# Kernel tuning notes

Hardware: AMD Instinct MI355X
Metric: run time of the kernel (lower is better)

Reference implementation:

```python
import jax, jax.numpy as jnp
import numpy as np

B, S, D, H, E, K = 4, 2048, 1024, 4096, 8, 2


def setup_inputs() -> dict:
    key = jax.random.key(0)
    ks = jax.random.split(key, 7)
    sd = 1.0 / np.sqrt(D)
    sh = 1.0 / np.sqrt(H)
    return {
        "x": jax.random.normal(ks[0], (B, S, D), dtype=jnp.float32),
        "Wg": jax.random.uniform(ks[1], (D, E), jnp.float32, -sd, sd),
        "bg": jnp.zeros((E,), jnp.float32),
        "W1": jax.random.uniform(ks[2], (E, D, H), jnp.float32, -sd, sd),
        "b1": jax.random.uniform(ks[3], (E, H), jnp.float32, -sd, sd),
        "W2": jax.random.uniform(ks[4], (E, H, D), jnp.float32, -sh, sh),
        "b2": jax.random.uniform(ks[5], (E, D), jnp.float32, -sh, sh),
    }


def reference(x, Wg, bg, W1, b1, W2, b2):
    # gating: softmax over experts, then top-k
    probs = jax.nn.softmax(x @ Wg + bg, axis=-1)            # [B,S,E]
    topv, topi = jax.lax.top_k(probs, K)                     # [B,S,K]
    # NOTE: original computes normalized scores but uses RAW top-k scores
    # scatter raw top-k scores back to dense per-expert weights [B,S,E]
    onehot = jax.nn.one_hot(topi, E, dtype=x.dtype)          # [B,S,K,E]
    w_dense = jnp.einsum("bske,bsk->bse", onehot, topv)      # [B,S,E]
    out = jnp.zeros_like(x)
    for e in range(E):
        h = jax.nn.relu(jnp.einsum("bsd,dh->bsh", x, W1[e]) + b1[e])
        y = jnp.einsum("bsh,hd->bsd", h, W2[e]) + b2[e]
        out = out + y * w_dense[..., e:e + 1]
    return out
```

## Files before the change

### kernel.cpp

```cpp
#include <hip/hip_runtime.h>

typedef unsigned short u16;
typedef __attribute__((ext_vector_type(8))) short bf16x8;
typedef __attribute__((ext_vector_type(8))) unsigned short u16x8;
typedef __attribute__((ext_vector_type(4))) float f32x4;

#define NTOK 8192
#define DDIM 1024
#define HDIM 4096
#define NEXP 8

typedef __attribute__((address_space(1))) const void gvoid;
typedef __attribute__((address_space(3))) void lvoid;

__device__ __forceinline__ u16 f2b(float f) {
  unsigned u = __float_as_uint(f);
  u += 0x7fffu + ((u >> 16) & 1u);
  return (u16)(u >> 16);
}
__device__ __forceinline__ void glds16(const void* g, void* l) {
  __builtin_amdgcn_global_load_lds((gvoid*)g, (lvoid*)l, 16, 0, 0);
}

__global__ void convert_x_kernel(const float* __restrict__ src, u16* __restrict__ dst) {
  size_t i = ((size_t)blockIdx.x * 256 + threadIdx.x) * 8;
  float4 a = *(const float4*)(src + i);
  float4 b = *(const float4*)(src + i + 4);
  u16x8 o;
  o[0] = f2b(a.x); o[1] = f2b(a.y); o[2] = f2b(a.z); o[3] = f2b(a.w);
  o[4] = f2b(b.x); o[5] = f2b(b.y); o[6] = f2b(b.z); o[7] = f2b(b.w);
  *(u16x8*)(dst + i) = o;
}

__global__ void transpose_kernel(const float* __restrict__ src, u16* __restrict__ dst,
                                 int R, int C) {
  int e = blockIdx.z;
  src += (size_t)e * R * C;
  dst += (size_t)e * R * C;
  int r0 = blockIdx.y * 64, c0 = blockIdx.x * 64;
  __shared__ u16 T[64][68];
  int t = threadIdx.x;
  int rr = t >> 4, cc = (t & 15) * 4;
#pragma unroll
  for (int i = 0; i < 4; ++i) {
    int r = i * 16 + rr;
    float4 v = *(const float4*)(src + (size_t)(r0 + r) * C + c0 + cc);
    T[cc + 0][r] = f2b(v.x);
    T[cc + 1][r] = f2b(v.y);
    T[cc + 2][r] = f2b(v.z);
    T[cc + 3][r] = f2b(v.w);
  }
  __syncthreads();
#pragma unroll
  for (int i = 0; i < 4; ++i) {
    int c = i * 16 + rr;
    ushort4 o = *(const ushort4*)&T[c][cc];
    *(ushort4*)(dst + (size_t)(c0 + c) * R + r0 + cc) = o;
  }
}

__global__ void gate_kernel(const float* __restrict__ x, const float* __restrict__ Wg,
                            const float* __restrict__ bg, int* __restrict__ counts_pad,
                            int* __restrict__ pair_tok, float* __restrict__ pair_w,
                            int* __restrict__ tok_ep)
{
  int lane = threadIdx.x & 63;
  int wave = threadIdx.x >> 6;
  int tok = blockIdx.x * 4 + wave;
  const float* xr = x + (size_t)tok * DDIM + lane * 16;
  float acc[NEXP];
#pragma unroll
  for (int e = 0; e < NEXP; ++e) acc[e] = 0.f;
#pragma unroll
  for (int j = 0; j < 16; ++j) {
    float xf = xr[j];
    const float* wr = Wg + (size_t)(lane * 16 + j) * NEXP;
    float4 wa = *(const float4*)(wr);
    float4 wb = *(const float4*)(wr + 4);
    acc[0] = fmaf(xf, wa.x, acc[0]);
    acc[1] = fmaf(xf, wa.y, acc[1]);
    acc[2] = fmaf(xf, wa.z, acc[2]);
    acc[3] = fmaf(xf, wa.w, acc[3]);
    acc[4] = fmaf(xf, wb.x, acc[4]);
    acc[5] = fmaf(xf, wb.y, acc[5]);
    acc[6] = fmaf(xf, wb.z, acc[6]);
    acc[7] = fmaf(xf, wb.w, acc[7]);
  }
#pragma unroll
  for (int off = 32; off > 0; off >>= 1) {
#pragma unroll
    for (int e = 0; e < NEXP; ++e) acc[e] += __shfl_xor(acc[e], off, 64);
  }
  if (lane == 0) {
    float l[NEXP];
    float mx = -3.4e38f;
#pragma unroll
    for (int e = 0; e < NEXP; ++e) { l[e] = acc[e] + bg[e]; mx = fmaxf(mx, l[e]); }
    float s = 0.f;
#pragma unroll
    for (int e = 0; e < NEXP; ++e) { l[e] = __expf(l[e] - mx); s += l[e]; }
    float inv = 1.f / s;
    float v1 = -1.f; int i1 = 0;
#pragma unroll
    for (int e = 0; e < NEXP; ++e) { if (l[e] > v1) { v1 = l[e]; i1 = e; } }
    float v2 = -1.f; int i2 = 0;
#pragma unroll
    for (int e = 0; e < NEXP; ++e) { if (e != i1 && l[e] > v2) { v2 = l[e]; i2 = e; } }
    int p1 = atomicAdd(&counts_pad[i1 * 32], 1);
    pair_tok[i1 * NTOK + p1] = tok;
    pair_w[i1 * NTOK + p1] = v1 * inv;
    tok_ep[2 * tok + 0] = (i1 << 16) | p1;
    int p2 = atomicAdd(&counts_pad[i2 * 32], 1);
    pair_tok[i2 * NTOK + p2] = tok;
    pair_w[i2 * NTOK + p2] = v2 * inv;
    tok_ep[2 * tok + 1] = (i2 << 16) | p2;
  }
}

__global__ void offsets_kernel(const int* __restrict__ counts_pad, int* __restrict__ counts,
                               int* __restrict__ offsets, int* __restrict__ tile_e,
                               int* __restrict__ tile_i0, int* __restrict__ ntiles)
{
  if (threadIdx.x == 0) {
    int s = 0;
    for (int e = 0; e < NEXP; ++e) {
      int c = counts_pad[e * 32];
      counts[e] = c; offsets[e] = s; s += c;
    }
    int nt_ = 0;
    for (int e = 0; e < NEXP; ++e)
      for (int i0 = 0; i0 < counts[e]; i0 += 128) { tile_e[nt_] = e; tile_i0[nt_] = i0; nt_++; }
    *ntiles = nt_;
  }
}

__device__ __forceinline__ void stage4(const u16* xa0, const u16* xa1,
                                       const u16* wb0, const u16* wb1,
                                       u16* Asb, u16* Bsb, int wave, int koff) {
  glds16(xa0 + koff, Asb + wave * 512);
  glds16(xa1 + koff, Asb + 2048 + wave * 512);
  glds16(wb0 + koff, Bsb + wave * 512);
  glds16(wb1 + koff, Bsb + 2048 + wave * 512);
}

__device__ __forceinline__ void mfma_tile(const u16* Asb, const u16* Bsb,
                                          f32x4 (&acc)[4][4],
                                          int wrr, int wc, int ln, int q) {
  bf16x8 af[4], bfr[4];
#pragma unroll
  for (int mt = 0; mt < 4; ++mt)
    af[mt] = *(const bf16x8*)(Asb + (wrr + mt * 16 + ln) * 32 + q * 8);
#pragma unroll
  for (int nt = 0; nt < 4; ++nt)
    bfr[nt] = *(const bf16x8*)(Bsb + (wc + nt * 16 + ln) * 32 + q * 8);
#pragma unroll
  for (int mt = 0; mt < 4; ++mt)
#pragma unroll
    for (int nt = 0; nt < 4; ++nt)
      acc[mt][nt] = __builtin_amdgcn_mfma_f32_16x16x32_bf16(af[mt], bfr[nt], acc[mt][nt], 0, 0, 0);
}

__global__ __launch_bounds__(256) void gemm1_kernel(
    const u16* __restrict__ xb, const u16* __restrict__ W1T,
    const float* __restrict__ b1, const int* __restrict__ counts,
    const int* __restrict__ offsets, const int* __restrict__ ntiles,
    const int* __restrict__ tile_e, const int* __restrict__ tile_i0,
    const int* __restrict__ pair_tok, u16* __restrict__ h, int hp, int p0)
{
  int bx = blockIdx.x;
  if (bx >= *ntiles) return;
  int e = tile_e[bx];
  int i0 = tile_i0[bx];
  int cnt = counts[e];
  int n0 = blockIdx.y * 128;

  __shared__ __align__(16) u16 As[2][128 * 32];
  __shared__ __align__(16) u16 Bs[2][128 * 32];

  int t = threadIdx.x;
  int lane = t & 63;
  int wave = t >> 6;
  int rlim = cnt - i0;
  int rl = rlim - 1;

  const int* tokp = pair_tok + e * NTOK + i0;
  int arow = t >> 2;
  int c8 = (t & 3) * 8;
  const u16* xa0 = xb + (size_t)tokp[min(arow, rl)] * DDIM + c8;
  const u16* xa1 = xb + (size_t)tokp[min(arow + 64, rl)] * DDIM + c8;
  const u16* wb0 = W1T + (size_t)e * HDIM * DDIM + (size_t)(p0 + n0 + arow) * DDIM + c8;
  const u16* wb1 = wb0 + (size_t)64 * DDIM;

  f32x4 acc[4][4] = {};
  int wrr = (wave >> 1) * 64;
  int wc = (wave & 1) * 64;
  int ln = lane & 15;
  int q = lane >> 4;

  stage4(xa0, xa1, wb0, wb1, As[0], Bs[0], wave, 0);
  __syncthreads();
  for (int k0 = 0; k0 < DDIM; k0 += 64) {
    stage4(xa0, xa1, wb0, wb1, As[1], Bs[1], wave, k0 + 32);
    __builtin_amdgcn_sched_barrier(0);
    mfma_tile(As[0], Bs[0], acc, wrr, wc, ln, q);
    __syncthreads();
    if (k0 + 64 < DDIM) {
      stage4(xa0, xa1, wb0, wb1, As[0], Bs[0], wave, k0 + 64);
      __builtin_amdgcn_sched_barrier(0);
    }
    mfma_tile(As[1], Bs[1], acc, wrr, wc, ln, q);
    __syncthreads();
  }

  int ob = offsets[e];
  float bb[4];
#pragma unroll
  for (int nt = 0; nt < 4; ++nt)
    bb[nt] = b1[(size_t)e * HDIM + p0 + n0 + wc + nt * 16 + ln];
  size_t hbase = (size_t)(ob + i0) * hp + n0 + wc;
#pragma unroll
  for (int mt = 0; mt < 4; ++mt) {
#pragma unroll
    for (int r = 0; r < 4; ++r) {
      int row = wrr + mt * 16 + q * 4 + r;
      if (row < rlim) {
        u16* hrow = h + hbase + (size_t)row * hp;
#pragma unroll
        for (int nt = 0; nt < 4; ++nt) {
          float v = acc[mt][nt][r] + bb[nt];
          hrow[nt * 16 + ln] = f2b(fmaxf(v, 0.f));
        }
      }
    }
  }
}

__global__ __launch_bounds__(256) void gemm2_kernel(
    const u16* __restrict__ h, const u16* __restrict__ W2T,
    const float* __restrict__ b2v, const int* __restrict__ counts,
    const int* __restrict__ offsets, const int* __restrict__ ntiles,
    const int* __restrict__ tile_e, const int* __restrict__ tile_i0,
    float* __restrict__ y, int hp, int p0, int first)
{
  int bx = blockIdx.x;
  if (bx >= *ntiles) return;
  int e = tile_e[bx];
  int i0 = tile_i0[bx];
  int cnt = counts[e];
  int n0 = blockIdx.y * 128;

  __shared__ __align__(16) u16 As[2][128 * 32];
  __shared__ __align__(16) u16 Bs[2][128 * 32];

  int t = threadIdx.x;
  int lane = t & 63;
  int wave = t >> 6;
  int rlim = cnt - i0;
  int rl = rlim - 1;
  int rbase = offsets[e] + i0;

  int arow = t >> 2;
  int c8 = (t & 3) * 8;
  const u16* xa0 = h + (size_t)(rbase + min(arow, rl)) * hp + c8;
  const u16* xa1 = h + (size_t)(rbase + min(arow + 64, rl)) * hp + c8;
  const u16* wb0 = W2T + (size_t)e * DDIM * HDIM + (size_t)(n0 + arow) * HDIM + p0 + c8;
  const u16* wb1 = wb0 + (size_t)64 * HDIM;

  f32x4 acc[4][4] = {};
  int wrr = (wave >> 1) * 64;
  int wc = (wave & 1) * 64;
  int ln = lane & 15;
  int q = lane >> 4;

  stage4(xa0, xa1, wb0, wb1, As[0], Bs[0], wave, 0);
  __syncthreads();
  for (int k0 = 0; k0 < hp; k0 += 64) {
    stage4(xa0, xa1, wb0, wb1, As[1], Bs[1], wave, k0 + 32);
    __builtin_amdgcn_sched_barrier(0);
    mfma_tile(As[0], Bs[0], acc, wrr, wc, ln, q);
    __syncthreads();
    if (k0 + 64 < hp) {
      stage4(xa0, xa1, wb0, wb1, As[0], Bs[0], wave, k0 + 64);
      __builtin_amdgcn_sched_barrier(0);
    }
    mfma_tile(As[1], Bs[1], acc, wrr, wc, ln, q);
    __syncthreads();
  }

  float bb[4];
#pragma unroll
  for (int nt = 0; nt < 4; ++nt)
    bb[nt] = first ? b2v[(size_t)e * DDIM + n0 + wc + nt * 16 + ln] : 0.f;
#pragma unroll
  for (int mt = 0; mt < 4; ++mt) {
#pragma unroll
    for (int r = 0; r < 4; ++r) {
      int row = wrr + mt * 16 + q * 4 + r;
      if (row < rlim) {
        float* yr = y + (size_t)(rbase + row) * DDIM + n0 + wc;
#pragma unroll
        for (int nt = 0; nt < 4; ++nt) {
          float v = acc[mt][nt][r] + bb[nt];
          if (first) yr[nt * 16 + ln] = v;
          else       yr[nt * 16 + ln] += v;
        }
      }
    }
  }
}

__global__ __launch_bounds__(256) void combine_kernel(
    const float* __restrict__ y, const int* __restrict__ tok_ep,
    const float* __restrict__ pair_w, const int* __restrict__ offsets,
    float* __restrict__ out)
{
  int tok = blockIdx.x;
  int ep1 = tok_ep[2 * tok + 0];
  int ep2 = tok_ep[2 * tok + 1];
  int e1 = ep1 >> 16, p1 = ep1 & 0xffff;
  int e2 = ep2 >> 16, p2 = ep2 & 0xffff;
  float w1 = pair_w[e1 * NTOK + p1];
  float w2 = pair_w[e2 * NTOK + p2];
  const float* r1 = y + (size_t)(offsets[e1] + p1) * DDIM;
  const float* r2 = y + (size_t)(offsets[e2] + p2) * DDIM;
  int c = threadIdx.x * 4;
  float4 a = *(const float4*)(r1 + c);
  float4 b = *(const float4*)(r2 + c);
  float4 o;
  o.x = w1 * a.x + w2 * b.x;
  o.y = w1 * a.y + w2 * b.y;
  o.z = w1 * a.z + w2 * b.z;
  o.w = w1 * a.w + w2 * b.w;
  *(float4*)(out + (size_t)tok * DDIM + c) = o;
}

extern "C" void kernel_launch(void* const* d_in, const int* in_sizes, int n_in,
                              void* d_out, int out_size, void* d_ws, size_t ws_size,
                              hipStream_t stream)
{
  const float* x  = (const float*)d_in[0];
  const float* Wg = (const float*)d_in[1];
  const float* bg = (const float*)d_in[2];
  const float* W1 = (const float*)d_in[3];
  const float* b1 = (const float*)d_in[4];
  const float* W2 = (const float*)d_in[5];
  const float* b2 = (const float*)d_in[6];
  float* out = (float*)d_out;

  char* ws = (char*)d_ws;
  int*   counts_pad = (int*)(ws + 0);
  int*   counts     = (int*)(ws + 1024);
  int*   offsets    = (int*)(ws + 1056);
  int*   ntiles     = (int*)(ws + 1088);
  int*   tile_e     = (int*)(ws + 1152);
  int*   tile_i0    = (int*)(ws + 2176);
  int*   tok_ep     = (int*)(ws + 4096);
  int*   pair_tok   = (int*)(ws + 69632);
  float* pair_w     = (float*)(ws + 331776);
  u16*   xb  = (u16*)(ws + 593920);
  u16*   W1T = (u16*)(ws + 593920 + 16777216);
  u16*   W2T = (u16*)(ws + 593920 + 16777216 + 67108864);
  float* yb  = (float*)(ws + 593920 + 16777216 + 2 * (size_t)67108864);
  u16*   hbuf = (u16*)(ws + 593920 + 16777216 + 3 * (size_t)67108864);
  size_t used_base = 593920 + 16777216 + 3 * (size_t)67108864;

  int hp = 256;
  const int cands[5] = {4096, 2048, 1024, 512, 256};
  for (int ci = 0; ci < 5; ++ci) {
    if (used_base + (size_t)16512 * cands[ci] * 2 <= ws_size) { hp = cands[ci]; break; }
  }

  hipMemsetAsync(counts_pad, 0, 1024, stream);
  convert_x_kernel<<<NTOK * DDIM / 2048, 256, 0, stream>>>(x, xb);
  transpose_kernel<<<dim3(HDIM / 64, DDIM / 64, NEXP), 256, 0, stream>>>(W1, W1T, DDIM, HDIM);
  transpose_kernel<<<dim3(DDIM / 64, HDIM / 64, NEXP), 256, 0, stream>>>(W2, W2T, HDIM, DDIM);
  gate_kernel<<<NTOK / 4, 256, 0, stream>>>(x, Wg, bg, counts_pad, pair_tok, pair_w, tok_ep);
  offsets_kernel<<<1, 64, 0, stream>>>(counts_pad, counts, offsets, tile_e, tile_i0, ntiles);
  for (int p0 = 0; p0 < HDIM; p0 += hp) {
    gemm1_kernel<<<dim3(136, hp / 128), 256, 0, stream>>>(
        xb, W1T, b1, counts, offsets, ntiles, tile_e, tile_i0, pair_tok, hbuf, hp, p0);
    gemm2_kernel<<<dim3(136, DDIM / 128), 256, 0, stream>>>(
        hbuf, W2T, b2, counts, offsets, ntiles, tile_e, tile_i0, yb, hp, p0, p0 == 0 ? 1 : 0);
  }
  combine_kernel<<<NTOK, 256, 0, stream>>>(yb, tok_ep, pair_w, offsets, out);
}
```

Measured before the change: 839.2 us.

## Triple-buffer GEMM K-loop with one barrier per step and interleave tile order

Replaces the double-buffered K loop in both expert GEMMs with a three-stage LDS ring. Each step waits on vmcnt so two loads stay in flight and uses a single s_barrier instead of two __syncthreads. The offsets kernel also permutes the tile list with a stride-17 interleave so blocks of different experts are mixed across the grid, marking padding slots with e=-1. This should hide global-to-LDS latency better and spread expert work more evenly, at the cost of 50% more LDS per block, which may lower occupancy.

```diff
diff --git a/kernel.cpp b/kernel.cpp
--- a/kernel.cpp
+++ b/kernel.cpp
@@ -9,6 +9,7 @@
 #define DDIM 1024
 #define HDIM 4096
 #define NEXP 8
+#define NTILE 136
 
 typedef __attribute__((address_space(1))) const void gvoid;
 typedef __attribute__((address_space(3))) void lvoid;
@@ -122,6 +123,7 @@
                                int* __restrict__ tile_i0, int* __restrict__ ntiles)
 {
   if (threadIdx.x == 0) {
+    int te[NTILE], ti[NTILE];
     int s = 0;
     for (int e = 0; e < NEXP; ++e) {
       int c = counts_pad[e * 32];
@@ -129,7 +131,12 @@
     }
     int nt_ = 0;
     for (int e = 0; e < NEXP; ++e)
-      for (int i0 = 0; i0 < counts[e]; i0 += 128) { tile_e[nt_] = e; tile_i0[nt_] = i0; nt_++; }
+      for (int i0 = 0; i0 < counts[e]; i0 += 128) { te[nt_] = e; ti[nt_] = i0; nt_++; }
+    for (int w = 0; w < NTILE; ++w) {
+      int t = (w & 7) * 17 + (w >> 3);
+      tile_e[w]  = (t < nt_) ? te[t] : -1;
+      tile_i0[w] = (t < nt_) ? ti[t] : 0;
+    }
     *ntiles = nt_;
   }
 }
@@ -160,6 +167,27 @@
       acc[mt][nt] = __builtin_amdgcn_mfma_f32_16x16x32_bf16(af[mt], bfr[nt], acc[mt][nt], 0, 0, 0);
 }
 
+#define GEMM_LOOP(KDIM)                                                      \
+  stage4(xa0, xa1, wb0, wb1, As[0], Bs[0], wave, 0);                         \
+  stage4(xa0, xa1, wb0, wb1, As[1], Bs[1], wave, 32);                        \
+  {                                                                          \
+    int cur = 0, nx2 = 2;                                                    \
+    for (int k0 = 0; k0 < (KDIM); k0 += 32) {                                \
+      __builtin_amdgcn_sched_barrier(0);                                     \
+      if (k0 + 32 < (KDIM))                                                  \
+        asm volatile("s_waitcnt vmcnt(4) lgkmcnt(0)" ::: "memory");          \
+      else                                                                   \
+        asm volatile("s_waitcnt vmcnt(0) lgkmcnt(0)" ::: "memory");          \
+      __builtin_amdgcn_s_barrier();                                          \
+      __builtin_amdgcn_sched_barrier(0);                                     \
+      if (k0 + 64 < (KDIM))                                                  \
+        stage4(xa0, xa1, wb0, wb1, As[nx2], Bs[nx2], wave, k0 + 64);         \
+      mfma_tile(As[cur], Bs[cur], acc, wrr, wc, ln, q);                      \
+      cur = (cur == 2) ? 0 : cur + 1;                                        \
+      nx2 = (nx2 == 2) ? 0 : nx2 + 1;                                        \
+    }                                                                        \
+  }
+
 __global__ __launch_bounds__(256) void gemm1_kernel(
     const u16* __restrict__ xb, const u16* __restrict__ W1T,
     const float* __restrict__ b1, const int* __restrict__ counts,
@@ -168,14 +196,14 @@
     const int* __restrict__ pair_tok, u16* __restrict__ h, int hp, int p0)
 {
   int bx = blockIdx.x;
-  if (bx >= *ntiles) return;
   int e = tile_e[bx];
+  if (e < 0) return;
   int i0 = tile_i0[bx];
   int cnt = counts[e];
   int n0 = blockIdx.y * 128;
 
-  __shared__ __align__(16) u16 As[2][128 * 32];
-  __shared__ __align__(16) u16 Bs[2][128 * 32];
+  __shared__ __align__(16) u16 As[3][4096];
+  __shared__ __align__(16) u16 Bs[3][4096];
 
   int t = threadIdx.x;
   int lane = t & 63;
@@ -197,20 +225,7 @@
   int ln = lane & 15;
   int q = lane >> 4;
 
-  stage4(xa0, xa1, wb0, wb1, As[0], Bs[0], wave, 0);
-  __syncthreads();
-  for (int k0 = 0; k0 < DDIM; k0 += 64) {
-    stage4(xa0, xa1, wb0, wb1, As[1], Bs[1], wave, k0 + 32);
-    __builtin_amdgcn_sched_barrier(0);
-    mfma_tile(As[0], Bs[0], acc, wrr, wc, ln, q);
-    __syncthreads();
-    if (k0 + 64 < DDIM) {
-      stage4(xa0, xa1, wb0, wb1, As[0], Bs[0], wave, k0 + 64);
-      __builtin_amdgcn_sched_barrier(0);
-    }
-    mfma_tile(As[1], Bs[1], acc, wrr, wc, ln, q);
-    __syncthreads();
-  }
+  GEMM_LOOP(DDIM);
 
   int ob = offsets[e];
   float bb[4];
@@ -243,14 +258,14 @@
     float* __restrict__ y, int hp, int p0, int first)
 {
   int bx = blockIdx.x;
-  if (bx >= *ntiles) return;
   int e = tile_e[bx];
+  if (e < 0) return;
   int i0 = tile_i0[bx];
   int cnt = counts[e];
   int n0 = blockIdx.y * 128;
 
-  __shared__ __align__(16) u16 As[2][128 * 32];
-  __shared__ __align__(16) u16 Bs[2][128 * 32];
+  __shared__ __align__(16) u16 As[3][4096];
+  __shared__ __align__(16) u16 Bs[3][4096];
 
   int t = threadIdx.x;
   int lane = t & 63;
@@ -272,20 +287,7 @@
   int ln = lane & 15;
   int q = lane >> 4;
 
-  stage4(xa0, xa1, wb0, wb1, As[0], Bs[0], wave, 0);
-  __syncthreads();
-  for (int k0 = 0; k0 < hp; k0 += 64) {
-    stage4(xa0, xa1, wb0, wb1, As[1], Bs[1], wave, k0 + 32);
-    __builtin_amdgcn_sched_barrier(0);
-    mfma_tile(As[0], Bs[0], acc, wrr, wc, ln, q);
-    __syncthreads();
-    if (k0 + 64 < hp) {
-      stage4(xa0, xa1, wb0, wb1, As[0], Bs[0], wave, k0 + 64);
-      __builtin_amdgcn_sched_barrier(0);
-    }
-    mfma_tile(As[1], Bs[1], acc, wrr, wc, ln, q);
-    __syncthreads();
-  }
+  GEMM_LOOP(hp);
 
   float bb[4];
 #pragma unroll
@@ -377,9 +379,9 @@
   gate_kernel<<<NTOK / 4, 256, 0, stream>>>(x, Wg, bg, counts_pad, pair_tok, pair_w, tok_ep);
   offsets_kernel<<<1, 64, 0, stream>>>(counts_pad, counts, offsets, tile_e, tile_i0, ntiles);
   for (int p0 = 0; p0 < HDIM; p0 += hp) {
-    gemm1_kernel<<<dim3(136, hp / 128), 256, 0, stream>>>(
+    gemm1_kernel<<<dim3(NTILE, hp / 128), 256, 0, stream>>>(
         xb, W1T, b1, counts, offsets, ntiles, tile_e, tile_i0, pair_tok, hbuf, hp, p0);
-    gemm2_kernel<<<dim3(136, DDIM / 128), 256, 0, stream>>>(
+    gemm2_kernel<<<dim3(NTILE, DDIM / 128), 256, 0, stream>>>(
         hbuf, W2T, b2, counts, offsets, ntiles, tile_e, tile_i0, yb, hp, p0, p0 == 0 ? 1 : 0);
   }
   combine_kernel<<<NTOK, 256, 0, stream>>>(yb, tok_ep, pair_w, offsets, out);
```

Result: slower. 917.3 us (+9.3%).
